# Performance work log

Measured on AMD Instinct MI355X. Metric: run time of the kernel, lower is better.

Reference implementation:

```python
import jax, jax.numpy as jnp
import numpy as np
from jax import lax

jax.config.update("jax_enable_x64", True)  # source casts distances to double for sinkhorn

N_E = 512
E_DIM = 256
NUM_EXPERTS = 10
B = 8192
MU = 0.25
BETA = 1.0
SK_EPS = 0.01
SK_ITERS = 100


def setup_inputs() -> dict:
    key = jax.random.key(0)
    k0, k1, k2, k3 = jax.random.split(key, 4)
    x = jax.random.normal(k0, (B, E_DIM), dtype=jnp.float32)
    label = jax.random.randint(k1, (N_E,), 0, 10)  # cluster id per code of codebook 0
    gate_probs = jax.random.uniform(k2, (B, NUM_EXPERTS), dtype=jnp.float32)
    # embeddings initialized uniform(-1/n_e, 1/n_e) as in __init__
    emb = jax.random.uniform(k3, (NUM_EXPERTS + 1, N_E, E_DIM), dtype=jnp.float32,
                             minval=-1.0 / N_E, maxval=1.0 / N_E)
    return {"x": x, "label": label, "idx": 0, "gate_probs": gate_probs, "emb": emb}


def _sinkhorn(d, eps, iters):
    # standard SwAV-style sinkhorn (as used in UniTok/LETTER); d: [B, K] float64
    logits = -d / eps
    Q = jnp.exp(logits - jnp.max(logits))  # max-shift is a no-op after global normalization
    Q = (Q / jnp.sum(Q)).T  # [K, B]
    K, Bn = Q.shape

    def step(Q, _):
        Q = Q / (jnp.sum(Q, axis=1, keepdims=True) * K)
        Q = Q / (jnp.sum(Q, axis=0, keepdims=True) * Bn)
        return Q, None

    Q, _ = lax.scan(step, Q, None, length=iters)
    return (Q * Bn).T  # [B, K]


def _assign(latent, W):
    d = (jnp.sum(latent ** 2, axis=1, keepdims=True)
         + jnp.sum(W ** 2, axis=1)[None, :]
         - 2.0 * latent @ W.T)  # [B, n_e]
    mx, mn = jnp.max(d), jnp.min(d)
    mid = (mx + mn) / 2
    amp = mx - mid + 1e-5
    d = ((d - mid) / amp).astype(jnp.float64)
    Q = _sinkhorn(d, SK_EPS, SK_ITERS)
    return jnp.argmax(Q, axis=-1)  # [B]


def reference(x, label, idx, gate_probs, emb):
    latent = x.reshape(-1, E_DIM)  # [B, D]
    nb = latent.shape[0]

    # per-expert sinkhorn assignment (use_sk=True, sk_epsilon>0 path)
    indices_all = jax.vmap(lambda W: _assign(latent, W))(emb)          # [11, B]
    xq_all = jax.vmap(lambda W, i: W[i])(emb, indices_all)              # [11, B, D]

    x_q = jnp.einsum('be,ebd->bd', gate_probs, xq_all[:NUM_EXPERTS])
    x_q = 0.95 * x_q + 0.05 * xq_all[NUM_EXPERTS]

    # diversity loss on codebook 0: positive = another code in the same cluster
    ind0 = indices_all[0]                      # [B]
    clusters = label[ind0]                     # [B]
    ar = jnp.arange(N_E)
    pos_mask = (label[None, :] == clusters[:, None]) & (ar[None, :] != ind0[:, None])
    y_true = jnp.argmax(pos_mask, axis=1)      # deterministic positive sample
    sim = x_q @ emb[0].T                       # [B, n_e]
    sim = sim.at[jnp.arange(nb), ind0].add(-1e12)  # mask self-similarity
    logp = jax.nn.log_softmax(sim, axis=-1)
    diversity_loss = -jnp.mean(logp[jnp.arange(nb), y_true])

    commitment_loss = jnp.mean((lax.stop_gradient(x_q) - x) ** 2)
    codebook_loss = jnp.mean((x_q - lax.stop_gradient(x)) ** 2)
    loss = codebook_loss + MU * commitment_loss + BETA * diversity_loss

    # selected index per token: codebook of top expert
    expert_id = jnp.argmax(gate_probs, axis=1)          # [B] in [0,10)
    indices = indices_all.T[jnp.arange(nb), expert_id]  # [B]

    x_q_out = x + lax.stop_gradient(x_q - x)  # straight-through
    return x_q_out, loss, indices
```

## Files before the change

kernel.cpp:

```cpp
#include <hip/hip_runtime.h>
#include <cstdint>
#include <cstddef>

#define NTOK 8192
#define NE 512
#define EDIM 256
#define NEXPALL 11
#define NITER 100

static __device__ __forceinline__ double wredsum(double x) {
  for (int o = 32; o > 0; o >>= 1) x += __shfl_down(x, o, 64);
  return x;
}

static constexpr double S32 = 2.3283064365386963e-10;
static constexpr double Q32 = 4294967296.0;

__global__ void k_init(unsigned* colmin, double* r0, double* uprev,
                       unsigned* dmaxA, unsigned* dminA, int* conv_iter, double* sums) {
  int i = blockIdx.x * 256 + threadIdx.x;
  if (i < NEXPALL * NTOK) colmin[i] = 0x7F800000u;
  if (i < NEXPALL * NE) { r0[i] = 0.0; uprev[i] = 0.0; }
  if (i < NEXPALL) { dmaxA[i] = 0u; dminA[i] = 0x7F800000u; conv_iter[i] = 1 << 30; }
  if (i < 2) sums[i] = 0.0;
}

__global__ __launch_bounds__(256) void k_npsq(const float* __restrict__ p, float* __restrict__ o, int rows) {
  int r = blockIdx.x * 16 + (threadIdx.x >> 4);
  int l = threadIdx.x & 15;
  if (r >= rows) return;
  const float* a = p + (size_t)r * EDIM;
  int leaf = l >> 3;
  int j = l & 7;
  const float* base = a + leaf * 128 + j;
  float acc = __fmul_rn(base[0], base[0]);
#pragma unroll
  for (int i = 8; i < 128; i += 8) {
    float v = base[i];
    acc = __fadd_rn(acc, __fmul_rn(v, v));
  }
  acc = __fadd_rn(acc, __shfl_xor(acc, 1, 64));
  acc = __fadd_rn(acc, __shfl_xor(acc, 2, 64));
  acc = __fadd_rn(acc, __shfl_xor(acc, 4, 64));
  float other = __shfl_xor(acc, 8, 64);
  float tot = (leaf == 0) ? __fadd_rn(acc, other) : __fadd_rn(other, acc);
  if (l == 0) o[r] = tot;
}

__global__ __launch_bounds__(256, 2) void k_gemm_d(const float* __restrict__ x, const float* __restrict__ emb,
                                                   const float* __restrict__ sx, const float* __restrict__ sw,
                                                   float* __restrict__ bigF,
                                                   unsigned* __restrict__ colminA,
                                                   unsigned* __restrict__ dmaxA,
                                                   unsigned* __restrict__ dminA) {
  int bx = blockIdx.x, by = blockIdx.y, e = blockIdx.z;
  int tid = threadIdx.x;
  int tx = tid & 15, ty = tid >> 4;
  int b0 = bx * 128, k0 = by * 128;

  __shared__ float xs[16][128];
  __shared__ float es[16][128];
  __shared__ float sxs[128];
  __shared__ float sws[128];
  __shared__ unsigned colm[128];
  __shared__ float wrx[4], wrn[4];

  if (tid < 128) { sxs[tid] = sx[b0 + tid]; colm[tid] = 0x7F800000u; }
  else { sws[tid - 128] = sw[e * NE + k0 + tid - 128]; }

  int lr = tid & 127;
  int lh = tid >> 7;
  const float* xrow = x + (size_t)(b0 + lr) * EDIM + lh * 8;
  const float* wrow = emb + ((size_t)e * NE + k0 + lr) * EDIM + lh * 8;

  float4 xa = *(const float4*)(xrow + 0);
  float4 xb = *(const float4*)(xrow + 4);
  float4 wa = *(const float4*)(wrow + 0);
  float4 wb = *(const float4*)(wrow + 4);

  float acc[8][8] = {};

  for (int kc = 0; kc < EDIM; kc += 16) {
    __syncthreads();
    xs[lh * 8 + 0][lr] = xa.x; xs[lh * 8 + 1][lr] = xa.y;
    xs[lh * 8 + 2][lr] = xa.z; xs[lh * 8 + 3][lr] = xa.w;
    xs[lh * 8 + 4][lr] = xb.x; xs[lh * 8 + 5][lr] = xb.y;
    xs[lh * 8 + 6][lr] = xb.z; xs[lh * 8 + 7][lr] = xb.w;
    es[lh * 8 + 0][lr] = wa.x; es[lh * 8 + 1][lr] = wa.y;
    es[lh * 8 + 2][lr] = wa.z; es[lh * 8 + 3][lr] = wa.w;
    es[lh * 8 + 4][lr] = wb.x; es[lh * 8 + 5][lr] = wb.y;
    es[lh * 8 + 6][lr] = wb.z; es[lh * 8 + 7][lr] = wb.w;
    __syncthreads();
    if (kc + 16 < EDIM) {
      xa = *(const float4*)(xrow + kc + 16);
      xb = *(const float4*)(xrow + kc + 20);
      wa = *(const float4*)(wrow + kc + 16);
      wb = *(const float4*)(wrow + kc + 20);
    }
#pragma unroll
    for (int kk = 0; kk < 16; ++kk) {
      float4 xv0 = *(const float4*)&xs[kk][tx * 4];
      float4 xv1 = *(const float4*)&xs[kk][64 + tx * 4];
      float4 wv0 = *(const float4*)&es[kk][ty * 4];
      float4 wv1 = *(const float4*)&es[kk][64 + ty * 4];
      float xr[8] = {xv0.x, xv0.y, xv0.z, xv0.w, xv1.x, xv1.y, xv1.z, xv1.w};
      float wr[8] = {wv0.x, wv0.y, wv0.z, wv0.w, wv1.x, wv1.y, wv1.z, wv1.w};
#pragma unroll
      for (int i = 0; i < 8; ++i)
#pragma unroll
        for (int j = 0; j < 8; ++j)
          acc[i][j] = fmaf(xr[i], wr[j], acc[i][j]);
    }
  }

  float dmx = -3.0e38f, dmn = 3.0e38f;
#pragma unroll
  for (int i = 0; i < 8; ++i) {
    int tokL = (i >> 2) * 64 + tx * 4 + (i & 3);
    float sxv = sxs[tokL];
    float cmin = 3.0e38f;
#pragma unroll
    for (int j = 0; j < 8; ++j) {
      int codeL = (j >> 2) * 64 + ty * 4 + (j & 3);
      float m2 = __fmul_rn(2.0f, acc[i][j]);
      float dv = __fsub_rn(__fadd_rn(sxv, sws[codeL]), m2);
      acc[i][j] = dv;
      dmx = fmaxf(dmx, dv); dmn = fminf(dmn, dv);
      cmin = fminf(cmin, dv);
    }
    atomicMin(&colm[tokL], __float_as_uint(cmin));
  }
  for (int o = 32; o > 0; o >>= 1) {
    dmx = fmaxf(dmx, __shfl_down(dmx, o, 64));
    dmn = fminf(dmn, __shfl_down(dmn, o, 64));
  }
  int wvi = tid >> 6, ln = tid & 63;
  if (ln == 0) { wrx[wvi] = dmx; wrn[wvi] = dmn; }
  __syncthreads();
  if (tid == 0) {
    float m1 = fmaxf(fmaxf(wrx[0], wrx[1]), fmaxf(wrx[2], wrx[3]));
    float m2 = fminf(fminf(wrn[0], wrn[1]), fminf(wrn[2], wrn[3]));
    atomicMax(dmaxA + e, __float_as_uint(m1));
    atomicMin(dminA + e, __float_as_uint(m2));
  }
  if (tid < 128) atomicMin(colminA + (size_t)e * NTOK + b0 + tid, colm[tid]);
#pragma unroll
  for (int j2 = 0; j2 < 2; ++j2)
#pragma unroll
    for (int cc = 0; cc < 4; ++cc) {
      int code = j2 * 64 + ty * 4 + cc;
      int cj = j2 * 4 + cc;
      float* ob = bigF + ((size_t)e * NE + k0 + code) * NTOK + b0;
      float4 lo = make_float4(acc[0][cj], acc[1][cj], acc[2][cj], acc[3][cj]);
      float4 hi = make_float4(acc[4][cj], acc[5][cj], acc[6][cj], acc[7][cj]);
      *(float4*)(ob + tx * 4) = lo;
      *(float4*)(ob + 64 + tx * 4) = hi;
    }
}

__global__ __launch_bounds__(256) void k_prep(const unsigned* __restrict__ colminA,
                                              const unsigned* __restrict__ dmaxA,
                                              const unsigned* __restrict__ dminA,
                                              double* __restrict__ cml, double* __restrict__ v) {
  int e = blockIdx.y;
  int b = blockIdx.x * 256 + threadIdx.x;
  float mx = __uint_as_float(dmaxA[e]);
  float mn = __uint_as_float(dminA[e]);
  float mid = __fmul_rn(__fadd_rn(mx, mn), 0.5f);
  float amp = __fadd_rn(__fsub_rn(mx, mid), 1e-5f);
  float cminf = __uint_as_float(colminA[(size_t)e * NTOK + b]);
  float dn = __fdiv_rn(__fsub_rn(cminf, mid), amp);
  double l = (-(double)dn) / 0.01;
  cml[(size_t)e * NTOK + b] = l;
  v[(size_t)e * NTOK + b] = exp(l);
}

__global__ __launch_bounds__(256) void k_build(float* __restrict__ bigF,
                                               const unsigned* __restrict__ dmaxA,
                                               const unsigned* __restrict__ dminA,
                                               const double* __restrict__ cml, const double* __restrict__ v0,
                                               double* __restrict__ r0) {
  int bx = blockIdx.x, k = blockIdx.y, e = blockIdx.z;
  int tid = threadIdx.x;
  float mx = __uint_as_float(dmaxA[e]);
  float mn = __uint_as_float(dminA[e]);
  float mid = __fmul_rn(__fadd_rn(mx, mn), 0.5f);
  float amp = __fadd_rn(__fsub_rn(mx, mid), 1e-5f);
  size_t rb = ((size_t)e * NE + k) * NTOK;
  int cb = bx * 2048 + tid * 8;
  float4 fa = *(const float4*)(bigF + rb + cb);
  float4 fb = *(const float4*)(bigF + rb + cb + 4);
  float din[8] = {fa.x, fa.y, fa.z, fa.w, fb.x, fb.y, fb.z, fb.w};
  unsigned qo[8];
  double racc = 0.0;
#pragma unroll
  for (int j = 0; j < 8; ++j) {
    int b = cb + j;
    float dn = __fdiv_rn(__fsub_rn(din[j], mid), amp);
    double l = (-(double)dn) / 0.01;
    double t = l - cml[(size_t)e * NTOK + b];
    double Bv = exp(t);
    double qd = (1.0 - Bv) * Q32;
    qd = fmin(fmax(qd, 0.0), 4294967295.0);
    unsigned q = (unsigned)llrint(qd);
    qo[j] = q;
    double Bq = fma(-(double)q, S32, 1.0);
    racc = fma(Bq, v0[(size_t)e * NTOK + b], racc);
  }
  uint4 oa = make_uint4(qo[0], qo[1], qo[2], qo[3]);
  uint4 ob2 = make_uint4(qo[4], qo[5], qo[6], qo[7]);
  *(uint4*)((unsigned*)bigF + rb + cb) = oa;
  *(uint4*)((unsigned*)bigF + rb + cb + 4) = ob2;
  racc = wredsum(racc);
  __shared__ double pr[4];
  int wv = tid >> 6, ln = tid & 63;
  if (ln == 0) pr[wv] = racc;
  __syncthreads();
  if (tid == 0) atomicAdd(&r0[e * NE + k], (pr[0] + pr[1]) + (pr[2] + pr[3]));
}

__global__ __launch_bounds__(256) void k_iter_f(const unsigned* __restrict__ bigU,
                                                const double* __restrict__ r0,
                                                double* __restrict__ rpart,
                                                double* __restrict__ uprev,
                                                int* __restrict__ conv_iter, int t) {
  int e = blockIdx.y, sub = blockIdx.x, tid = threadIdx.x;
  if (t > ((volatile int*)conv_iter)[e]) return;
  __shared__ double us[NE];
  __shared__ double vloc[256];
  __shared__ int okf;
  if (tid == 0) okf = 1;
  size_t ebase = (size_t)e * NE * NTOK;
  const double* rp_e = rpart + (size_t)e * 32 * NE;
  double* rp_mine = rpart + ((size_t)e * 32 + sub) * NE;

  int k2 = tid * 2;
  double s0, s1;
  if (t == 1) {
    s0 = r0[e * NE + k2];
    s1 = r0[e * NE + k2 + 1];
  } else {
    s0 = 0.0; s1 = 0.0;
    for (int j = 0; j < 32; ++j) {
      s0 += rp_e[(size_t)j * NE + k2];
      s1 += rp_e[(size_t)j * NE + k2 + 1];
    }
  }
  double u0 = 1.0 / (512.0 * s0);
  double u1 = 1.0 / (512.0 * s1);
  us[k2] = u0; us[k2 + 1] = u1;
  __syncthreads();
  if (sub == 0) {
    double p0 = uprev[e * NE + k2], p1 = uprev[e * NE + k2 + 1];
    bool ok = (fabs(u0 - p0) <= 1e-13 * fabs(u0)) && (fabs(u1 - p1) <= 1e-13 * fabs(u1));
    if (!ok) okf = 0;
    uprev[e * NE + k2] = u0; uprev[e * NE + k2 + 1] = u1;
  }
  __syncthreads();
  if (sub == 0 && tid == 0 && okf) atomicMin(conv_iter + e, t);

  int col = sub * 256 + tid;
  const unsigned* cp = bigU + ebase + col;
  double c0 = 0, c1 = 0, c2 = 0, c3 = 0;
#pragma unroll 2
  for (int k = 0; k < NE; k += 4) {
    unsigned q0 = cp[(size_t)(k + 0) * NTOK];
    unsigned q1 = cp[(size_t)(k + 1) * NTOK];
    unsigned q2 = cp[(size_t)(k + 2) * NTOK];
    unsigned q3 = cp[(size_t)(k + 3) * NTOK];
    c0 = fma(us[k + 0], fma(-(double)q0, S32, 1.0), c0);
    c1 = fma(us[k + 1], fma(-(double)q1, S32, 1.0), c1);
    c2 = fma(us[k + 2], fma(-(double)q2, S32, 1.0), c2);
    c3 = fma(us[k + 3], fma(-(double)q3, S32, 1.0), c3);
  }
  double c = (c0 + c1) + (c2 + c3);
  vloc[tid] = 1.0 / (8192.0 * c);
  __syncthreads();

  int wv = tid >> 6, ln = tid & 63;
  int cb = sub * 256 + ln * 4;
  double vv0 = vloc[ln * 4 + 0], vv1 = vloc[ln * 4 + 1];
  double vv2 = vloc[ln * 4 + 2], vv3 = vloc[ln * 4 + 3];
  for (int k = wv; k < NE; k += 4) {
    const unsigned* rp = bigU + ebase + (size_t)k * NTOK + cb;
    uint4 qa = *(const uint4*)rp;
    double p;
    p = vv0 * fma(-(double)qa.x, S32, 1.0);
    p = fma(vv1, fma(-(double)qa.y, S32, 1.0), p);
    p = fma(vv2, fma(-(double)qa.z, S32, 1.0), p);
    p = fma(vv3, fma(-(double)qa.w, S32, 1.0), p);
    p = wredsum(p);
    if (ln == 0) rp_mine[k] = p;
  }
}

__global__ __launch_bounds__(256) void k_final(const unsigned* __restrict__ bigU,
                                               const double* __restrict__ rpart,
                                               int* __restrict__ idxs) {
  int e = blockIdx.y, sub = blockIdx.x, tid = threadIdx.x;
  __shared__ double us[NE];
  const double* rp_e = rpart + (size_t)e * 32 * NE;
  int k2 = tid * 2;
  double s0 = 0.0, s1 = 0.0;
  for (int j = 0; j < 32; ++j) {
    s0 += rp_e[(size_t)j * NE + k2];
    s1 += rp_e[(size_t)j * NE + k2 + 1];
  }
  us[k2] = 1.0 / (512.0 * s0);
  us[k2 + 1] = 1.0 / (512.0 * s1);
  __syncthreads();
  int col = sub * 256 + tid;
  const unsigned* cp = bigU + (size_t)e * NE * NTOK + col;
  double best = -1.0;
  int bi = 0;
#pragma unroll 4
  for (int k = 0; k < NE; ++k) {
    double s = us[k] * fma(-(double)cp[(size_t)k * NTOK], S32, 1.0);
    if (s > best) { best = s; bi = k; }
  }
  idxs[(size_t)e * NTOK + col] = bi;
}

__global__ __launch_bounds__(256) void k_mix(const float* __restrict__ x, const float* __restrict__ gate,
                                             const float* __restrict__ emb, const int* __restrict__ idxs,
                                             float* __restrict__ xq, float* __restrict__ out0,
                                             float* __restrict__ outIdx, double* __restrict__ mse_sum) {
  int tid = threadIdx.x;
  int sub = tid >> 5, lane = tid & 31;
  int tok = blockIdx.x * 8 + sub;
  float acc[8] = {0, 0, 0, 0, 0, 0, 0, 0};
#pragma unroll
  for (int ee = 0; ee < 10; ++ee) {
    int id = idxs[(size_t)ee * NTOK + tok];
    float g = gate[tok * 10 + ee];
    const float* er = emb + ((size_t)ee * NE + id) * EDIM + lane;
#pragma unroll
    for (int dd = 0; dd < 8; ++dd) acc[dd] = fmaf(g, er[32 * dd], acc[dd]);
  }
  int id10 = idxs[(size_t)10 * NTOK + tok];
  const float* es = emb + ((size_t)10 * NE + id10) * EDIM + lane;
  double ms = 0.0;
#pragma unroll
  for (int dd = 0; dd < 8; ++dd) {
    int d = lane + 32 * dd;
    float q = 0.95f * acc[dd] + 0.05f * es[32 * dd];
    float xv = x[(size_t)tok * EDIM + d];
    float df = q - xv;
    out0[(size_t)tok * EDIM + d] = xv + df;
    xq[(size_t)tok * EDIM + d] = q;
    ms += (double)df * (double)df;
  }
  ms = wredsum(ms);
  __shared__ double pr[4];
  int wv = tid >> 6, ln = tid & 63;
  if (ln == 0) pr[wv] = ms;
  __syncthreads();
  if (tid == 0) atomicAdd(mse_sum, (pr[0] + pr[1]) + (pr[2] + pr[3]));
  if (lane == 0) {
    const float* gr = gate + tok * 10;
    float bg = gr[0];
    int be = 0;
#pragma unroll
    for (int ee = 1; ee < 10; ++ee) { float g = gr[ee]; if (g > bg) { bg = g; be = ee; } }
    outIdx[tok] = (float)idxs[(size_t)be * NTOK + tok];
  }
}

__global__ __launch_bounds__(256, 2) void k_simgemm(const float* __restrict__ xq, const float* __restrict__ emb,
                                                    float* __restrict__ sim) {
  int bx = blockIdx.x, by = blockIdx.y, tid = threadIdx.x;
  int tx = tid & 15, ty = tid >> 4;
  int b0 = bx * 128, j0 = by * 128;
  __shared__ float xs[16][128];
  __shared__ float es[16][128];
  int lr = tid & 127;
  int lh = tid >> 7;
  const float* xrow = xq + (size_t)(b0 + lr) * EDIM + lh * 8;
  const float* erow = emb + (size_t)(j0 + lr) * EDIM + lh * 8;
  float4 xa = *(const float4*)(xrow + 0);
  float4 xb = *(const float4*)(xrow + 4);
  float4 wa = *(const float4*)(erow + 0);
  float4 wb = *(const float4*)(erow + 4);
  float acc[8][8] = {};
  for (int kc = 0; kc < EDIM; kc += 16) {
    __syncthreads();
    xs[lh * 8 + 0][lr] = xa.x; xs[lh * 8 + 1][lr] = xa.y;
    xs[lh * 8 + 2][lr] = xa.z; xs[lh * 8 + 3][lr] = xa.w;
    xs[lh * 8 + 4][lr] = xb.x; xs[lh * 8 + 5][lr] = xb.y;
    xs[lh * 8 + 6][lr] = xb.z; xs[lh * 8 + 7][lr] = xb.w;
    es[lh * 8 + 0][lr] = wa.x; es[lh * 8 + 1][lr] = wa.y;
    es[lh * 8 + 2][lr] = wa.z; es[lh * 8 + 3][lr] = wa.w;
    es[lh * 8 + 4][lr] = wb.x; es[lh * 8 + 5][lr] = wb.y;
    es[lh * 8 + 6][lr] = wb.z; es[lh * 8 + 7][lr] = wb.w;
    __syncthreads();
    if (kc + 16 < EDIM) {
      xa = *(const float4*)(xrow + kc + 16);
      xb = *(const float4*)(xrow + kc + 20);
      wa = *(const float4*)(erow + kc + 16);
      wb = *(const float4*)(erow + kc + 20);
    }
#pragma unroll
    for (int kk = 0; kk < 16; ++kk) {
      float4 xv0 = *(const float4*)&xs[kk][ty * 4];
      float4 xv1 = *(const float4*)&xs[kk][64 + ty * 4];
      float4 wv0 = *(const float4*)&es[kk][tx * 4];
      float4 wv1 = *(const float4*)&es[kk][64 + tx * 4];
      float xr[8] = {xv0.x, xv0.y, xv0.z, xv0.w, xv1.x, xv1.y, xv1.z, xv1.w};
      float wr[8] = {wv0.x, wv0.y, wv0.z, wv0.w, wv1.x, wv1.y, wv1.z, wv1.w};
#pragma unroll
      for (int i = 0; i < 8; ++i)
#pragma unroll
        for (int j = 0; j < 8; ++j)
          acc[i][j] = fmaf(xr[i], wr[j], acc[i][j]);
    }
  }
#pragma unroll
  for (int i = 0; i < 8; ++i) {
    int tok = (i >> 2) * 64 + ty * 4 + (i & 3);
    float* ob = sim + (size_t)(b0 + tok) * NE + j0;
    float4 lo = make_float4(acc[i][0], acc[i][1], acc[i][2], acc[i][3]);
    float4 hi = make_float4(acc[i][4], acc[i][5], acc[i][6], acc[i][7]);
    *(float4*)(ob + tx * 4) = lo;
    *(float4*)(ob + 64 + tx * 4) = hi;
  }
}

__global__ __launch_bounds__(256) void k_div(const float* __restrict__ sim, const int* __restrict__ idxs,
                                             const int* __restrict__ label, double* __restrict__ div_sum) {
  __shared__ int lab[NE];
  int tid = threadIdx.x;
  lab[tid] = label[tid];
  lab[256 + tid] = label[256 + tid];
  __syncthreads();
  int wv = tid >> 6, ln = tid & 63;
  int b = blockIdx.x * 4 + wv;
  int ind0 = idxs[b];
  int clu = lab[ind0];
  const float* sr = sim + (size_t)b * NE;
  double vals[8];
  double mx = -1e300;
  int ys = 1024;
#pragma unroll
  for (int c = 0; c < 8; ++c) {
    int j = ln + 64 * c;
    double vv = (double)sr[j];
    if (j == ind0) vv -= 1e12;
    vals[c] = vv;
    mx = fmax(mx, vv);
    if (lab[j] == clu && j != ind0 && j < ys) ys = j;
  }
  for (int o = 32; o > 0; o >>= 1) {
    mx = fmax(mx, __shfl_xor(mx, o, 64));
    ys = min(ys, __shfl_xor(ys, o, 64));
  }
  int y = (ys >= 1024) ? 0 : ys;
  double se = 0.0, vy = 0.0;
#pragma unroll
  for (int c = 0; c < 8; ++c) {
    int j = ln + 64 * c;
    se += exp(vals[c] - mx);
    if (j == y) vy = vals[c];
  }
  for (int o = 32; o > 0; o >>= 1) {
    se += __shfl_xor(se, o, 64);
    vy += __shfl_xor(vy, o, 64);
  }
  if (ln == 0) {
    double lse = mx + log(se);
    atomicAdd(div_sum, lse - vy);
  }
}

__global__ void k_loss(const double* __restrict__ sums, float* __restrict__ out) {
  double mse = sums[0] / 2097152.0;
  double dv = sums[1] / 8192.0;
  double loss = (mse + 0.25 * mse) + dv;
  out[0] = (float)loss;
}

extern "C" void kernel_launch(void* const* d_in, const int* in_sizes, int n_in,
                              void* d_out, int out_size, void* d_ws, size_t ws_size,
                              hipStream_t stream) {
  (void)in_sizes; (void)n_in; (void)out_size;
  const float* x = (const float*)d_in[0];
  const int* label = (const int*)d_in[1];
  const float* gate = (const float*)d_in[3];
  const float* emb = (const float*)d_in[4];
  float* out = (float*)d_out;
  float* out0 = out;
  float* outLoss = out + (size_t)NTOK * EDIM;
  float* outIdx = out + (size_t)NTOK * EDIM + 1;

  char* w = (char*)d_ws;
  size_t off = 0;
  auto alloc = [&](size_t bytes) -> void* {
    void* p = w + off;
    off += (bytes + 15) & ~(size_t)15;
    return p;
  };
  float* bigF = (float*)alloc((size_t)NEXPALL * NE * NTOK * 4);
  unsigned* bigU = (unsigned*)bigF;
  float* sim = (float*)bigF;
  unsigned* colminA = (unsigned*)alloc((size_t)NEXPALL * NTOK * 4);
  double* cml = (double*)alloc((size_t)NEXPALL * NTOK * 8);
  double* v = (double*)alloc((size_t)NEXPALL * NTOK * 8);
  double* r0 = (double*)alloc((size_t)NEXPALL * NE * 8);
  double* rpart = (double*)alloc((size_t)NEXPALL * 32 * NE * 8);
  double* uprev = (double*)alloc((size_t)NEXPALL * NE * 8);
  float* sxF = (float*)alloc((size_t)NTOK * 4);
  float* swF = (float*)alloc((size_t)NEXPALL * NE * 4);
  unsigned* dmaxA = (unsigned*)alloc(NEXPALL * 4);
  unsigned* dminA = (unsigned*)alloc(NEXPALL * 4);
  int* conv_iter = (int*)alloc(NEXPALL * 4);
  int* idxs = (int*)alloc((size_t)NEXPALL * NTOK * 4);
  float* xq = (float*)alloc((size_t)NTOK * EDIM * 4);
  double* sums = (double*)alloc(2 * 8);
  if (off > ws_size) return;

  k_init<<<352, 256, 0, stream>>>(colminA, r0, uprev, dmaxA, dminA, conv_iter, sums);
  k_npsq<<<NTOK / 16, 256, 0, stream>>>(x, sxF, NTOK);
  k_npsq<<<(NEXPALL * NE) / 16, 256, 0, stream>>>(emb, swF, NEXPALL * NE);
  k_gemm_d<<<dim3(64, 4, NEXPALL), 256, 0, stream>>>(x, emb, sxF, swF, bigF, colminA, dmaxA, dminA);
  k_prep<<<dim3(32, NEXPALL), 256, 0, stream>>>(colminA, dmaxA, dminA, cml, v);
  k_build<<<dim3(4, NE, NEXPALL), 256, 0, stream>>>(bigF, dmaxA, dminA, cml, v, r0);
  for (int t = 1; t <= NITER - 1; ++t)
    k_iter_f<<<dim3(32, NEXPALL), 256, 0, stream>>>(bigU, r0, rpart, uprev, conv_iter, t);
  k_final<<<dim3(32, NEXPALL), 256, 0, stream>>>(bigU, rpart, idxs);
  k_mix<<<NTOK / 8, 256, 0, stream>>>(x, gate, emb, idxs, xq, out0, outIdx, sums);
  k_simgemm<<<dim3(64, 4), 256, 0, stream>>>(xq, emb, sim);
  k_div<<<NTOK / 4, 256, 0, stream>>>(sim, idxs, label, sums + 1);
  k_loss<<<1, 1, 0, stream>>>(sums, outLoss);
}
```

Baseline: 1.340 ms.

## Split Sinkhorn iteration into separate column-sum and row-sum kernels

The fused Sinkhorn iteration kernel becomes two launches per iteration. A column-sum kernel computes v from the row scalings, and a row-sum kernel computes full row sums over all tokens, which removes the 32-way partial-sum buffer and its re-reduction. Both kernels, and the final argmax, now use 64 blocks per expert and split the reduction dimension across two halves of the block to raise parallelism. The cost is twice as many kernel launches per iteration, and v is now passed through global memory between the two launches.

```diff
diff --git a/kernel.cpp b/kernel.cpp
--- a/kernel.cpp
+++ b/kernel.cpp
@@ -219,35 +219,20 @@
   if (tid == 0) atomicAdd(&r0[e * NE + k], (pr[0] + pr[1]) + (pr[2] + pr[3]));
 }
 
-__global__ __launch_bounds__(256) void k_iter_f(const unsigned* __restrict__ bigU,
-                                                const double* __restrict__ r0,
-                                                double* __restrict__ rpart,
+__global__ __launch_bounds__(256) void k_colsum(const unsigned* __restrict__ bigU,
+                                                const double* __restrict__ rsrc,
+                                                double* __restrict__ vout,
                                                 double* __restrict__ uprev,
                                                 int* __restrict__ conv_iter, int t) {
   int e = blockIdx.y, sub = blockIdx.x, tid = threadIdx.x;
   if (t > ((volatile int*)conv_iter)[e]) return;
   __shared__ double us[NE];
-  __shared__ double vloc[256];
+  __shared__ double part[256];
   __shared__ int okf;
   if (tid == 0) okf = 1;
-  size_t ebase = (size_t)e * NE * NTOK;
-  const double* rp_e = rpart + (size_t)e * 32 * NE;
-  double* rp_mine = rpart + ((size_t)e * 32 + sub) * NE;
-
   int k2 = tid * 2;
-  double s0, s1;
-  if (t == 1) {
-    s0 = r0[e * NE + k2];
-    s1 = r0[e * NE + k2 + 1];
-  } else {
-    s0 = 0.0; s1 = 0.0;
-    for (int j = 0; j < 32; ++j) {
-      s0 += rp_e[(size_t)j * NE + k2];
-      s1 += rp_e[(size_t)j * NE + k2 + 1];
-    }
-  }
-  double u0 = 1.0 / (512.0 * s0);
-  double u1 = 1.0 / (512.0 * s1);
+  double u0 = 1.0 / (512.0 * rsrc[e * NE + k2]);
+  double u1 = 1.0 / (512.0 * rsrc[e * NE + k2 + 1]);
   us[k2] = u0; us[k2 + 1] = u1;
   __syncthreads();
   if (sub == 0) {
@@ -259,11 +244,13 @@
   __syncthreads();
   if (sub == 0 && tid == 0 && okf) atomicMin(conv_iter + e, t);
 
-  int col = sub * 256 + tid;
-  const unsigned* cp = bigU + ebase + col;
+  int lcol = tid & 127, half = tid >> 7;
+  int col = sub * 128 + lcol;
+  const unsigned* cp = bigU + (size_t)e * NE * NTOK + col;
+  int kh = half * 256;
   double c0 = 0, c1 = 0, c2 = 0, c3 = 0;
-#pragma unroll 2
-  for (int k = 0; k < NE; k += 4) {
+#pragma unroll 4
+  for (int k = kh; k < kh + 256; k += 4) {
     unsigned q0 = cp[(size_t)(k + 0) * NTOK];
     unsigned q1 = cp[(size_t)(k + 1) * NTOK];
     unsigned q2 = cp[(size_t)(k + 2) * NTOK];
@@ -273,52 +260,75 @@
     c2 = fma(us[k + 2], fma(-(double)q2, S32, 1.0), c2);
     c3 = fma(us[k + 3], fma(-(double)q3, S32, 1.0), c3);
   }
-  double c = (c0 + c1) + (c2 + c3);
-  vloc[tid] = 1.0 / (8192.0 * c);
-  __syncthreads();
-
+  part[tid] = (c0 + c1) + (c2 + c3);
+  __syncthreads();
+  if (tid < 128)
+    vout[(size_t)e * NTOK + sub * 128 + tid] = 1.0 / (8192.0 * (part[tid] + part[tid + 128]));
+}
+
+__global__ __launch_bounds__(256) void k_rowsum(const unsigned* __restrict__ bigU,
+                                                const double* __restrict__ v,
+                                                double* __restrict__ racc,
+                                                const int* __restrict__ conv_iter, int t) {
+  int e = blockIdx.y, sub = blockIdx.x, tid = threadIdx.x;
+  if (t > ((volatile int*)conv_iter)[e]) return;
+  size_t ebase = (size_t)e * NE * NTOK;
+  const double* vb = v + (size_t)e * NTOK;
+  double p[8] = {0, 0, 0, 0, 0, 0, 0, 0};
+  for (int i = 0; i < 8; ++i) {
+    int c = i * 1024 + tid * 4;
+    double2 va = *(const double2*)(vb + c);
+    double2 vc = *(const double2*)(vb + c + 2);
+#pragma unroll
+    for (int kk = 0; kk < 8; ++kk) {
+      const unsigned* rp = bigU + ebase + (size_t)(sub * 8 + kk) * NTOK + c;
+      uint4 q = *(const uint4*)rp;
+      p[kk] = fma(va.x, fma(-(double)q.x, S32, 1.0), p[kk]);
+      p[kk] = fma(va.y, fma(-(double)q.y, S32, 1.0), p[kk]);
+      p[kk] = fma(vc.x, fma(-(double)q.z, S32, 1.0), p[kk]);
+      p[kk] = fma(vc.y, fma(-(double)q.w, S32, 1.0), p[kk]);
+    }
+  }
+  __shared__ double pr[8][4];
   int wv = tid >> 6, ln = tid & 63;
-  int cb = sub * 256 + ln * 4;
-  double vv0 = vloc[ln * 4 + 0], vv1 = vloc[ln * 4 + 1];
-  double vv2 = vloc[ln * 4 + 2], vv3 = vloc[ln * 4 + 3];
-  for (int k = wv; k < NE; k += 4) {
-    const unsigned* rp = bigU + ebase + (size_t)k * NTOK + cb;
-    uint4 qa = *(const uint4*)rp;
-    double p;
-    p = vv0 * fma(-(double)qa.x, S32, 1.0);
-    p = fma(vv1, fma(-(double)qa.y, S32, 1.0), p);
-    p = fma(vv2, fma(-(double)qa.z, S32, 1.0), p);
-    p = fma(vv3, fma(-(double)qa.w, S32, 1.0), p);
-    p = wredsum(p);
-    if (ln == 0) rp_mine[k] = p;
-  }
+#pragma unroll
+  for (int kk = 0; kk < 8; ++kk) {
+    double s = wredsum(p[kk]);
+    if (ln == 0) pr[kk][wv] = s;
+  }
+  __syncthreads();
+  if (tid < 8)
+    racc[e * NE + sub * 8 + tid] = (pr[tid][0] + pr[tid][1]) + (pr[tid][2] + pr[tid][3]);
 }
 
 __global__ __launch_bounds__(256) void k_final(const unsigned* __restrict__ bigU,
-                                               const double* __restrict__ rpart,
+                                               const double* __restrict__ racc,
                                                int* __restrict__ idxs) {
   int e = blockIdx.y, sub = blockIdx.x, tid = threadIdx.x;
   __shared__ double us[NE];
-  const double* rp_e = rpart + (size_t)e * 32 * NE;
+  __shared__ double bv[256];
+  __shared__ int bix[256];
   int k2 = tid * 2;
-  double s0 = 0.0, s1 = 0.0;
-  for (int j = 0; j < 32; ++j) {
-    s0 += rp_e[(size_t)j * NE + k2];
-    s1 += rp_e[(size_t)j * NE + k2 + 1];
-  }
-  us[k2] = 1.0 / (512.0 * s0);
-  us[k2 + 1] = 1.0 / (512.0 * s1);
-  __syncthreads();
-  int col = sub * 256 + tid;
+  us[k2] = 1.0 / (512.0 * racc[e * NE + k2]);
+  us[k2 + 1] = 1.0 / (512.0 * racc[e * NE + k2 + 1]);
+  __syncthreads();
+  int lcol = tid & 127, half = tid >> 7;
+  int col = sub * 128 + lcol;
   const unsigned* cp = bigU + (size_t)e * NE * NTOK + col;
   double best = -1.0;
   int bi = 0;
+  int kh = half * 256;
 #pragma unroll 4
-  for (int k = 0; k < NE; ++k) {
+  for (int k = kh; k < kh + 256; ++k) {
     double s = us[k] * fma(-(double)cp[(size_t)k * NTOK], S32, 1.0);
     if (s > best) { best = s; bi = k; }
   }
-  idxs[(size_t)e * NTOK + col] = bi;
+  bv[tid] = best; bix[tid] = bi;
+  __syncthreads();
+  if (tid < 128) {
+    int r = (bv[tid + 128] > bv[tid]) ? bix[tid + 128] : bix[tid];
+    idxs[(size_t)e * NTOK + col] = r;
+  }
 }
 
 __global__ __launch_bounds__(256) void k_mix(const float* __restrict__ x, const float* __restrict__ gate,
@@ -505,7 +515,7 @@
   double* cml = (double*)alloc((size_t)NEXPALL * NTOK * 8);
   double* v = (double*)alloc((size_t)NEXPALL * NTOK * 8);
   double* r0 = (double*)alloc((size_t)NEXPALL * NE * 8);
-  double* rpart = (double*)alloc((size_t)NEXPALL * 32 * NE * 8);
+  double* racc = (double*)alloc((size_t)NEXPALL * NE * 8);
   double* uprev = (double*)alloc((size_t)NEXPALL * NE * 8);
   float* sxF = (float*)alloc((size_t)NTOK * 4);
   float* swF = (float*)alloc((size_t)NEXPALL * NE * 4);
@@ -523,9 +533,12 @@
   k_gemm_d<<<dim3(64, 4, NEXPALL), 256, 0, stream>>>(x, emb, sxF, swF, bigF, colminA, dmaxA, dminA);
   k_prep<<<dim3(32, NEXPALL), 256, 0, stream>>>(colminA, dmaxA, dminA, cml, v);
   k_build<<<dim3(4, NE, NEXPALL), 256, 0, stream>>>(bigF, dmaxA, dminA, cml, v, r0);
-  for (int t = 1; t <= NITER - 1; ++t)
-    k_iter_f<<<dim3(32, NEXPALL), 256, 0, stream>>>(bigU, r0, rpart, uprev, conv_iter, t);
-  k_final<<<dim3(32, NEXPALL), 256, 0, stream>>>(bigU, rpart, idxs);
+  for (int t = 1; t <= NITER - 1; ++t) {
+    const double* rsrc = (t == 1) ? r0 : racc;
+    k_colsum<<<dim3(64, NEXPALL), 256, 0, stream>>>(bigU, rsrc, v, uprev, conv_iter, t);
+    k_rowsum<<<dim3(64, NEXPALL), 256, 0, stream>>>(bigU, v, racc, conv_iter, t);
+  }
+  k_final<<<dim3(64, NEXPALL), 256, 0, stream>>>(bigU, racc, idxs);
   k_mix<<<NTOK / 8, 256, 0, stream>>>(x, gate, emb, idxs, xq, out0, outIdx, sums);
   k_simgemm<<<dim3(64, 4), 256, 0, stream>>>(xq, emb, sim);
   k_div<<<NTOK / 4, 256, 0, stream>>>(sim, idxs, label, sums + 1);
```

Measured after the change: 1.236 ms (median of 2 runs). 7.7% less time.
